# Kernel tuning notes

Hardware: AMD Instinct MI355X
Metric: run time of the kernel (lower is better)

Reference implementation:

```python
import jax, jax.numpy as jnp
import numpy as np

N = 100000   # nodes
E = 1250000  # edges
D = 64       # in = hidden = out channels
LN_EPS = 1e-5
L2_EPS = 1e-12


def setup_inputs() -> dict:
    key = jax.random.key(0)
    ks = jax.random.split(key, 16)
    s = 1.0 / np.sqrt(D)
    inp = {
        "x": jax.random.normal(ks[0], (N, D), jnp.float32),
        "edge_index": jax.random.randint(ks[1], (2, E), 0, N, dtype=jnp.int64),
    }
    for i in range(3):  # SAGEConv i: out = mean_aggr @ Wl + bl + x @ Wr
        inp[f"Wl{i}"] = jax.random.normal(ks[2 + 2 * i], (D, D), jnp.float32) * s
        inp[f"bl{i}"] = jnp.zeros((D,), jnp.float32)
        inp[f"Wr{i}"] = jax.random.normal(ks[3 + 2 * i], (D, D), jnp.float32) * s
    for i in range(2):  # LayerNorm after layers 0,1
        inp[f"g{i}"] = jnp.ones((D,), jnp.float32)
        inp[f"b{i}"] = jnp.zeros((D,), jnp.float32)
    return inp


def _sage_conv(x, src, dst, Wl, bl, Wr):
    # PyG SAGEConv(aggr='mean'): lin_l(mean of neighbor msgs) + lin_r(x)
    agg = jax.ops.segment_sum(x[src], dst, num_segments=N)          # [N, D]
    deg = jax.ops.segment_sum(jnp.ones((src.shape[0],), x.dtype), dst, num_segments=N)
    mean = agg / jnp.maximum(deg, 1.0)[:, None]
    return mean @ Wl + bl + x @ Wr


def _layer_norm(h, g, b):
    mu = jnp.mean(h, axis=-1, keepdims=True)
    var = jnp.mean((h - mu) ** 2, axis=-1, keepdims=True)
    return (h - mu) * jax.lax.rsqrt(var + LN_EPS) * g + b


def reference(x, edge_index, Wl0, bl0, Wr0, Wl1, bl1, Wr1, Wl2, bl2, Wr2, g0, b0, g1, b1):
    src, dst = edge_index[0], edge_index[1]
    Ws = [(Wl0, bl0, Wr0), (Wl1, bl1, Wr1), (Wl2, bl2, Wr2)]
    lns = [(g0, b0), (g1, b1)]
    h = x
    for i in range(3):
        res = h  # residual projections are Identity (equal dims)
        h = _sage_conv(h, src, dst, *Ws[i])
        if i < 2:
            h = _layer_norm(h, *lns[i])
            h = jax.nn.relu(h)
            h = h + res
            # dropout is identity in eval mode
        else:
            h = h + res
    # F.normalize(p=2, dim=1)
    nrm = jnp.sqrt(jnp.sum(h * h, axis=1, keepdims=True))
    return h / jnp.maximum(nrm, L2_EPS)
```

## Files before the change

kernel.cpp:

```cpp
#include <hip/hip_runtime.h>

#define DD   64
#define KK   128
#define XSTR 132
#define BSH  9
#define BNODES 512
#define BCAPSH 13

typedef unsigned int uint32;

__device__ __forceinline__ unsigned short f2bf_rne(float f) {
    uint32 u = __float_as_uint(f);
    u += 0x7fffu + ((u >> 16) & 1u);
    return (unsigned short)(u >> 16);
}
__device__ __forceinline__ float bf_lo(uint32 w) { return __uint_as_float(w << 16); }
__device__ __forceinline__ float bf_hi(uint32 w) { return __uint_as_float(w & 0xffff0000u); }

__global__ __launch_bounds__(256) void cvt_kernel(const float* __restrict__ x,
                                                  unsigned short* __restrict__ xb,
                                                  int n4, int* __restrict__ gCnt) {
    if (blockIdx.x == 0 && threadIdx.x < 256) gCnt[threadIdx.x] = 0;
    int i = blockIdx.x * 256 + threadIdx.x;
    if (i < n4) {
        float4 v = ((const float4*)x)[i];
        ushort4 p;
        p.x = f2bf_rne(v.x); p.y = f2bf_rne(v.y);
        p.z = f2bf_rne(v.z); p.w = f2bf_rne(v.w);
        ((ushort4*)xb)[i] = p;
    }
}

__global__ __launch_bounds__(1024) void bucket_kernel(const int* __restrict__ src,
                                                      const int* __restrict__ dst,
                                                      int* __restrict__ gCnt,
                                                      int2* __restrict__ buf, int E) {
    __shared__ int ldsCnt[256];
    __shared__ int base[256];
    const int t = threadIdx.x;
    if (t < 256) ldsCnt[t] = 0;
    __syncthreads();

    const int e0 = blockIdx.x * 4096;
    int bk[4], rk[4], sv[4], dv[4];
#pragma unroll
    for (int k = 0; k < 4; ++k) {
        int e = e0 + k * 1024 + t;
        bk[k] = -1;
        if (e < E) {
            dv[k] = dst[e];
            sv[k] = src[e];
            bk[k] = dv[k] >> BSH;
            rk[k] = atomicAdd(&ldsCnt[bk[k]], 1);
        }
    }
    __syncthreads();
    if (t < 256 && ldsCnt[t] > 0) base[t] = atomicAdd(&gCnt[t], ldsCnt[t]);
    __syncthreads();
#pragma unroll
    for (int k = 0; k < 4; ++k) {
        if (bk[k] >= 0) {
            int pos = (bk[k] << BCAPSH) + base[bk[k]] + rk[k];
            buf[pos] = make_int2(sv[k], dv[k]);
        }
    }
}

__global__ __launch_bounds__(256) void scan_buckets(const int* __restrict__ gCnt,
                                                    int* __restrict__ csrBase, int NB) {
    __shared__ int s[256];
    int t = threadIdx.x;
    int v = (t < NB) ? gCnt[t] : 0;
    s[t] = v;
    __syncthreads();
    for (int d = 1; d < 256; d <<= 1) {
        int u = (t >= d) ? s[t - d] : 0;
        __syncthreads();
        if (t >= d) s[t] += u;
        __syncthreads();
    }
    if (t < NB) csrBase[t] = s[t] - v;
}

__global__ __launch_bounds__(512) void csr_build(const int2* __restrict__ buf,
                                                 const int* __restrict__ gCnt,
                                                 const int* __restrict__ csrBase,
                                                 int* __restrict__ offsets,
                                                 int* __restrict__ csr, int N, int E) {
    __shared__ int c1[BNODES];
    __shared__ int s[BNODES];
    const int b = blockIdx.x;
    const int t = threadIdx.x;
    c1[t] = 0;
    __syncthreads();

    const int cnt = gCnt[b];
    const int2* bb = buf + ((size_t)b << BCAPSH);
    for (int i = t; i < cnt; i += 512) atomicAdd(&c1[bb[i].y & (BNODES - 1)], 1);
    __syncthreads();

    int v = c1[t];
    s[t] = v;
    __syncthreads();
    for (int d = 1; d < BNODES; d <<= 1) {
        int u = (t >= d) ? s[t - d] : 0;
        __syncthreads();
        if (t >= d) s[t] += u;
        __syncthreads();
    }
    int excl = s[t] - v;
    const int base = csrBase[b];
    const int node = (b << BSH) + t;
    if (node < N) offsets[node] = base + excl;
    if (b == 0 && t == 0) offsets[N] = E;
    __syncthreads();
    s[t] = excl;
    c1[t] = 0;
    __syncthreads();

    for (int i = t; i < cnt; i += 512) {
        int2 e = bb[i];
        int d = e.y & (BNODES - 1);
        int r = atomicAdd(&c1[d], 1);
        csr[base + s[d] + r] = e.x;
    }
}

__global__ __launch_bounds__(256) void aggregate_kernel(
    const unsigned short* __restrict__ hb,
    const int* __restrict__ offsets,
    const int* __restrict__ csr,
    float* __restrict__ agg,
    int N) {
    int node = (blockIdx.x * 256 + threadIdx.x) >> 3;
    if (node >= N) return;
    const int q = threadIdx.x & 7;

    const int off0 = offsets[node];
    const int off1 = offsets[node + 1];

    float a0 = 0.f, a1 = 0.f, a2 = 0.f, a3 = 0.f,
          a4 = 0.f, a5 = 0.f, a6 = 0.f, a7 = 0.f;

    for (int j = off0; j < off1; j += 8) {
        uint4 v[8];
#pragma unroll
        for (int s = 0; s < 8; ++s) {
            uint4 t = make_uint4(0u, 0u, 0u, 0u);
            int idx = j + s;
            if (idx < off1) {
                int sn = __builtin_nontemporal_load(&csr[idx]);
                t = ((const uint4*)(hb + (size_t)sn * DD))[q];
            }
            v[s] = t;
        }
#pragma unroll
        for (int s = 0; s < 8; ++s) {
            a0 += bf_lo(v[s].x); a1 += bf_hi(v[s].x);
            a2 += bf_lo(v[s].y); a3 += bf_hi(v[s].y);
            a4 += bf_lo(v[s].z); a5 += bf_hi(v[s].z);
            a6 += bf_lo(v[s].w); a7 += bf_hi(v[s].w);
        }
    }
    float invd = 1.0f / fmaxf((float)(off1 - off0), 1.0f);
    float4 lo = make_float4(a0 * invd, a1 * invd, a2 * invd, a3 * invd);
    float4 hi = make_float4(a4 * invd, a5 * invd, a6 * invd, a7 * invd);
    *(float4*)(&agg[(size_t)node * DD + q * 8])     = lo;
    *(float4*)(&agg[(size_t)node * DD + q * 8 + 4]) = hi;
}

template <int MODE>
__global__ __launch_bounds__(256) void node_update(
    const float* __restrict__ h,
    const float* __restrict__ mean,
    const float* __restrict__ Wl,
    const float* __restrict__ bl,
    const float* __restrict__ Wr,
    const float* __restrict__ g,
    const float* __restrict__ b,
    float* __restrict__ out,
    unsigned short* __restrict__ outb,
    int nNodes) {
    __shared__ float sW[KK * DD];
    __shared__ float sX[64 * XSTR];
    __shared__ float sbl[DD], sg[DD], sb[DD];

    const int t = threadIdx.x;

    for (int i = t; i < DD * DD; i += 256) {
        sW[i]           = Wl[i];
        sW[DD * DD + i] = Wr[i];
    }
    if (t < DD) {
        sbl[t] = bl[t];
        if (MODE == 0) { sg[t] = g[t]; sb[t] = b[t]; }
    }

    const int nbase = blockIdx.x * 64;

    for (int r = 0; r < 8; ++r) {
        int idx  = r * 256 + t;
        int node = idx >> 5;
        int q    = idx & 31;
        int n    = nbase + node;
        float4 v = make_float4(0.f, 0.f, 0.f, 0.f);
        if (n < nNodes) {
            v = (q < 16) ? ((const float4*)(mean + (size_t)n * DD))[q]
                         : ((const float4*)(h    + (size_t)n * DD))[q - 16];
        }
        *(float4*)(&sX[node * XSTR + q * 4]) = v;
    }
    __syncthreads();

    const int c0 = (t & 15) * 4;
    const int n0 = (t >> 4) * 4;

    float acc[4][4];
#pragma unroll
    for (int i = 0; i < 4; ++i)
#pragma unroll
        for (int j = 0; j < 4; ++j) acc[i][j] = sbl[c0 + j];

#pragma unroll 8
    for (int k = 0; k < KK; ++k) {
        const float4 w = *(const float4*)(&sW[k * DD + c0]);
#pragma unroll
        for (int i = 0; i < 4; ++i) {
            float xv = sX[(n0 + i) * XSTR + k];
            acc[i][0] = fmaf(xv, w.x, acc[i][0]);
            acc[i][1] = fmaf(xv, w.y, acc[i][1]);
            acc[i][2] = fmaf(xv, w.z, acc[i][2]);
            acc[i][3] = fmaf(xv, w.w, acc[i][3]);
        }
    }

    float res[4][4];
#pragma unroll
    for (int i = 0; i < 4; ++i) {
        float4 rv = *(const float4*)(&sX[(n0 + i) * XSTR + 64 + c0]);
        res[i][0] = rv.x; res[i][1] = rv.y; res[i][2] = rv.z; res[i][3] = rv.w;
    }

#pragma unroll
    for (int i = 0; i < 4; ++i) {
        int nn = nbase + n0 + i;
        float4 o;
        if (MODE == 0) {
            float s = acc[i][0] + acc[i][1] + acc[i][2] + acc[i][3];
            s += __shfl_xor(s, 1, 64);
            s += __shfl_xor(s, 2, 64);
            s += __shfl_xor(s, 4, 64);
            s += __shfl_xor(s, 8, 64);
            float mu = s * (1.0f / 64.0f);
            float d0 = acc[i][0] - mu, d1 = acc[i][1] - mu,
                  d2 = acc[i][2] - mu, d3 = acc[i][3] - mu;
            float qq = d0 * d0 + d1 * d1 + d2 * d2 + d3 * d3;
            qq += __shfl_xor(qq, 1, 64);
            qq += __shfl_xor(qq, 2, 64);
            qq += __shfl_xor(qq, 4, 64);
            qq += __shfl_xor(qq, 8, 64);
            float rstd = rsqrtf(qq * (1.0f / 64.0f) + 1e-5f);
            o.x = fmaxf(d0 * rstd * sg[c0 + 0] + sb[c0 + 0], 0.f) + res[i][0];
            o.y = fmaxf(d1 * rstd * sg[c0 + 1] + sb[c0 + 1], 0.f) + res[i][1];
            o.z = fmaxf(d2 * rstd * sg[c0 + 2] + sb[c0 + 2], 0.f) + res[i][2];
            o.w = fmaxf(d3 * rstd * sg[c0 + 3] + sb[c0 + 3], 0.f) + res[i][3];
        } else {
            float y0 = acc[i][0] + res[i][0], y1 = acc[i][1] + res[i][1],
                  y2 = acc[i][2] + res[i][2], y3 = acc[i][3] + res[i][3];
            float qq = y0 * y0 + y1 * y1 + y2 * y2 + y3 * y3;
            qq += __shfl_xor(qq, 1, 64);
            qq += __shfl_xor(qq, 2, 64);
            qq += __shfl_xor(qq, 4, 64);
            qq += __shfl_xor(qq, 8, 64);
            float inv = 1.0f / fmaxf(sqrtf(qq), 1e-12f);
            o.x = y0 * inv; o.y = y1 * inv; o.z = y2 * inv; o.w = y3 * inv;
        }
        if (nn < nNodes) {
            *(float4*)(&out[(size_t)nn * DD + c0]) = o;
            if (MODE == 0) {
                ushort4 p;
                p.x = f2bf_rne(o.x); p.y = f2bf_rne(o.y);
                p.z = f2bf_rne(o.z); p.w = f2bf_rne(o.w);
                *(ushort4*)(&outb[(size_t)nn * DD + c0]) = p;
            }
        }
    }
}

extern "C" void kernel_launch(void* const* d_in, const int* in_sizes, int n_in,
                              void* d_out, int out_size, void* d_ws, size_t ws_size,
                              hipStream_t stream) {
    const float* x   = (const float*)d_in[0];
    const int*   ei  = (const int*)d_in[1];
    const float* Wl0 = (const float*)d_in[2];
    const float* bl0 = (const float*)d_in[3];
    const float* Wr0 = (const float*)d_in[4];
    const float* Wl1 = (const float*)d_in[5];
    const float* bl1 = (const float*)d_in[6];
    const float* Wr1 = (const float*)d_in[7];
    const float* Wl2 = (const float*)d_in[8];
    const float* bl2 = (const float*)d_in[9];
    const float* Wr2 = (const float*)d_in[10];
    const float* g0  = (const float*)d_in[11];
    const float* b0  = (const float*)d_in[12];
    const float* g1  = (const float*)d_in[13];
    const float* b1  = (const float*)d_in[14];

    const int N = in_sizes[0] / DD;
    const int E = in_sizes[1] / 2;
    const int* src = ei;
    const int* dst = ei + E;
    const int NB = (N + BNODES - 1) >> BSH;

    float* A       = (float*)d_ws;
    float* B       = A + (size_t)N * DD;
    float* AGG     = B + (size_t)N * DD;
    int2*  bucketBuf = (int2*)A;
    unsigned short* HB = (unsigned short*)(AGG + (size_t)N * DD);
    int*   offsets = (int*)(HB + (size_t)N * DD);
    int*   gCnt    = offsets + (N + 1);
    int*   csrBase = gCnt + 256;
    int*   csr     = csrBase + 256;
    float* out     = (float*)d_out;

    const int tiles = (N + 63) / 64;
    const int agrid = (N + 31) / 32;
    const int n4    = N * DD / 4;
    const int cgrid = (n4 + 255) / 256;
    const int bgrid = (E + 4095) / 4096;

    cvt_kernel<<<cgrid, 256, 0, stream>>>(x, HB, n4, gCnt);
    bucket_kernel<<<bgrid, 1024, 0, stream>>>(src, dst, gCnt, bucketBuf, E);
    scan_buckets<<<1, 256, 0, stream>>>(gCnt, csrBase, NB);
    csr_build<<<NB, 512, 0, stream>>>(bucketBuf, gCnt, csrBase, offsets, csr, N, E);

    aggregate_kernel<<<agrid, 256, 0, stream>>>(HB, offsets, csr, AGG, N);
    node_update<0><<<tiles, 256, 0, stream>>>(x, AGG, Wl0, bl0, Wr0, g0, b0, A, HB, N);

    aggregate_kernel<<<agrid, 256, 0, stream>>>(HB, offsets, csr, AGG, N);
    node_update<0><<<tiles, 256, 0, stream>>>(A, AGG, Wl1, bl1, Wr1, g1, b1, B, HB, N);

    aggregate_kernel<<<agrid, 256, 0, stream>>>(HB, offsets, csr, AGG, N);
    node_update<1><<<tiles, 256, 0, stream>>>(B, AGG, Wl2, bl2, Wr2, nullptr, nullptr, out, nullptr, N);
}
```

Measured before the change: 373.8 us.

## Use bf16 MFMA in node update and store aggregated means as bf16

```diff
diff --git a/kernel.cpp b/kernel.cpp
--- a/kernel.cpp
+++ b/kernel.cpp
@@ -1,13 +1,14 @@
 #include <hip/hip_runtime.h>
 
 #define DD   64
-#define KK   128
-#define XSTR 132
+#define WSTR 136
 #define BSH  9
 #define BNODES 512
 #define BCAPSH 13
 
 typedef unsigned int uint32;
+typedef __attribute__((ext_vector_type(8))) short short8;
+typedef __attribute__((ext_vector_type(4))) float f32x4;
 
 __device__ __forceinline__ unsigned short f2bf_rne(float f) {
     uint32 u = __float_as_uint(f);
@@ -130,7 +131,7 @@
     const unsigned short* __restrict__ hb,
     const int* __restrict__ offsets,
     const int* __restrict__ csr,
-    float* __restrict__ agg,
+    unsigned short* __restrict__ aggb,
     int N) {
     int node = (blockIdx.x * 256 + threadIdx.x) >> 3;
     if (node >= N) return;
@@ -163,16 +164,21 @@
         }
     }
     float invd = 1.0f / fmaxf((float)(off1 - off0), 1.0f);
-    float4 lo = make_float4(a0 * invd, a1 * invd, a2 * invd, a3 * invd);
-    float4 hi = make_float4(a4 * invd, a5 * invd, a6 * invd, a7 * invd);
-    *(float4*)(&agg[(size_t)node * DD + q * 8])     = lo;
-    *(float4*)(&agg[(size_t)node * DD + q * 8 + 4]) = hi;
+    unsigned short* orow = aggb + (size_t)node * DD + q * 8;
+    ushort4 pa, pb;
+    pa.x = f2bf_rne(a0 * invd); pa.y = f2bf_rne(a1 * invd);
+    pa.z = f2bf_rne(a2 * invd); pa.w = f2bf_rne(a3 * invd);
+    pb.x = f2bf_rne(a4 * invd); pb.y = f2bf_rne(a5 * invd);
+    pb.z = f2bf_rne(a6 * invd); pb.w = f2bf_rne(a7 * invd);
+    *(ushort4*)(orow)     = pa;
+    *(ushort4*)(orow + 4) = pb;
 }
 
 template <int MODE>
-__global__ __launch_bounds__(256) void node_update(
+__global__ __launch_bounds__(256, 4) void node_update(
     const float* __restrict__ h,
-    const float* __restrict__ mean,
+    const unsigned short* __restrict__ meanb,
+    const unsigned short* __restrict__ hb,
     const float* __restrict__ Wl,
     const float* __restrict__ bl,
     const float* __restrict__ Wr,
@@ -181,107 +187,105 @@
     float* __restrict__ out,
     unsigned short* __restrict__ outb,
     int nNodes) {
-    __shared__ float sW[KK * DD];
-    __shared__ float sX[64 * XSTR];
+    __shared__ unsigned short sWt[64 * WSTR];
     __shared__ float sbl[DD], sg[DD], sb[DD];
 
     const int t = threadIdx.x;
 
-    for (int i = t; i < DD * DD; i += 256) {
-        sW[i]           = Wl[i];
-        sW[DD * DD + i] = Wr[i];
+    for (int idx = t; idx < 2 * DD * DD; idx += 256) {
+        int k = idx >> 6, c = idx & 63;
+        float v = (k < DD) ? Wl[idx] : Wr[idx - DD * DD];
+        sWt[c * WSTR + k] = f2bf_rne(v);
     }
     if (t < DD) {
         sbl[t] = bl[t];
         if (MODE == 0) { sg[t] = g[t]; sb[t] = b[t]; }
     }
-
-    const int nbase = blockIdx.x * 64;
-
-    for (int r = 0; r < 8; ++r) {
-        int idx  = r * 256 + t;
-        int node = idx >> 5;
-        int q    = idx & 31;
-        int n    = nbase + node;
-        float4 v = make_float4(0.f, 0.f, 0.f, 0.f);
-        if (n < nNodes) {
-            v = (q < 16) ? ((const float4*)(mean + (size_t)n * DD))[q]
-                         : ((const float4*)(h    + (size_t)n * DD))[q - 16];
-        }
-        *(float4*)(&sX[node * XSTR + q * 4]) = v;
-    }
-    __syncthreads();
-
-    const int c0 = (t & 15) * 4;
-    const int n0 = (t >> 4) * 4;
-
-    float acc[4][4];
-#pragma unroll
-    for (int i = 0; i < 4; ++i)
-#pragma unroll
-        for (int j = 0; j < 4; ++j) acc[i][j] = sbl[c0 + j];
-
-#pragma unroll 8
-    for (int k = 0; k < KK; ++k) {
-        const float4 w = *(const float4*)(&sW[k * DD + c0]);
-#pragma unroll
-        for (int i = 0; i < 4; ++i) {
-            float xv = sX[(n0 + i) * XSTR + k];
-            acc[i][0] = fmaf(xv, w.x, acc[i][0]);
-            acc[i][1] = fmaf(xv, w.y, acc[i][1]);
-            acc[i][2] = fmaf(xv, w.z, acc[i][2]);
-            acc[i][3] = fmaf(xv, w.w, acc[i][3]);
-        }
-    }
-
+    __syncthreads();
+
+    const int wave = t >> 6;
+    const int lane = t & 63;
+    const int quad = lane >> 4;
+    const int n16  = lane & 15;
+    const int nbase = blockIdx.x * 64 + wave * 16;
+
+    const int arow = min(nbase + n16, nNodes - 1);
+    const unsigned short* mrow = meanb + (size_t)arow * DD;
+    const unsigned short* hrow = hb    + (size_t)arow * DD;
+    short8 af[4];
+    af[0] = *(const short8*)(mrow + quad * 8);
+    af[1] = *(const short8*)(mrow + 32 + quad * 8);
+    af[2] = *(const short8*)(hrow + quad * 8);
+    af[3] = *(const short8*)(hrow + 32 + quad * 8);
+
+    const int rbase = nbase + quad * 4;
     float res[4][4];
 #pragma unroll
     for (int i = 0; i < 4; ++i) {
-        float4 rv = *(const float4*)(&sX[(n0 + i) * XSTR + 64 + c0]);
-        res[i][0] = rv.x; res[i][1] = rv.y; res[i][2] = rv.z; res[i][3] = rv.w;
+        int rr = min(rbase + i, nNodes - 1);
+#pragma unroll
+        for (int j = 0; j < 4; ++j)
+            res[i][j] = h[(size_t)rr * DD + j * 16 + n16];
+    }
+
+    f32x4 acc[4];
+#pragma unroll
+    for (int j = 0; j < 4; ++j) {
+        float bv = sbl[j * 16 + n16];
+        acc[j] = (f32x4){bv, bv, bv, bv};
+    }
+
+#pragma unroll
+    for (int s = 0; s < 4; ++s) {
+#pragma unroll
+        for (int j = 0; j < 4; ++j) {
+            short8 bf = *(const short8*)(&sWt[(j * 16 + n16) * WSTR + s * 32 + quad * 8]);
+            acc[j] = __builtin_amdgcn_mfma_f32_16x16x32_bf16(af[s], bf, acc[j], 0, 0, 0);
+        }
     }
 
 #pragma unroll
     for (int i = 0; i < 4; ++i) {
-        int nn = nbase + n0 + i;
-        float4 o;
+        int rr = rbase + i;
+        float o[4];
         if (MODE == 0) {
-            float s = acc[i][0] + acc[i][1] + acc[i][2] + acc[i][3];
-            s += __shfl_xor(s, 1, 64);
-            s += __shfl_xor(s, 2, 64);
-            s += __shfl_xor(s, 4, 64);
-            s += __shfl_xor(s, 8, 64);
-            float mu = s * (1.0f / 64.0f);
-            float d0 = acc[i][0] - mu, d1 = acc[i][1] - mu,
-                  d2 = acc[i][2] - mu, d3 = acc[i][3] - mu;
+            float s4 = acc[0][i] + acc[1][i] + acc[2][i] + acc[3][i];
+            s4 += __shfl_xor(s4, 1, 64);
+            s4 += __shfl_xor(s4, 2, 64);
+            s4 += __shfl_xor(s4, 4, 64);
+            s4 += __shfl_xor(s4, 8, 64);
+            float mu = s4 * (1.0f / 64.0f);
+            float d0 = acc[0][i] - mu, d1 = acc[1][i] - mu,
+                  d2 = acc[2][i] - mu, d3 = acc[3][i] - mu;
             float qq = d0 * d0 + d1 * d1 + d2 * d2 + d3 * d3;
             qq += __shfl_xor(qq, 1, 64);
             qq += __shfl_xor(qq, 2, 64);
             qq += __shfl_xor(qq, 4, 64);
             qq += __shfl_xor(qq, 8, 64);
             float rstd = rsqrtf(qq * (1.0f / 64.0f) + 1e-5f);
-            o.x = fmaxf(d0 * rstd * sg[c0 + 0] + sb[c0 + 0], 0.f) + res[i][0];
-            o.y = fmaxf(d1 * rstd * sg[c0 + 1] + sb[c0 + 1], 0.f) + res[i][1];
-            o.z = fmaxf(d2 * rstd * sg[c0 + 2] + sb[c0 + 2], 0.f) + res[i][2];
-            o.w = fmaxf(d3 * rstd * sg[c0 + 3] + sb[c0 + 3], 0.f) + res[i][3];
+            o[0] = fmaxf(d0 * rstd * sg[0 * 16 + n16] + sb[0 * 16 + n16], 0.f) + res[i][0];
+            o[1] = fmaxf(d1 * rstd * sg[1 * 16 + n16] + sb[1 * 16 + n16], 0.f) + res[i][1];
+            o[2] = fmaxf(d2 * rstd * sg[2 * 16 + n16] + sb[2 * 16 + n16], 0.f) + res[i][2];
+            o[3] = fmaxf(d3 * rstd * sg[3 * 16 + n16] + sb[3 * 16 + n16], 0.f) + res[i][3];
         } else {
-            float y0 = acc[i][0] + res[i][0], y1 = acc[i][1] + res[i][1],
-                  y2 = acc[i][2] + res[i][2], y3 = acc[i][3] + res[i][3];
-            float qq = y0 * y0 + y1 * y1 + y2 * y2 + y3 * y3;
+            o[0] = acc[0][i] + res[i][0];
+            o[1] = acc[1][i] + res[i][1];
+            o[2] = acc[2][i] + res[i][2];
+            o[3] = acc[3][i] + res[i][3];
+            float qq = o[0] * o[0] + o[1] * o[1] + o[2] * o[2] + o[3] * o[3];
             qq += __shfl_xor(qq, 1, 64);
             qq += __shfl_xor(qq, 2, 64);
             qq += __shfl_xor(qq, 4, 64);
             qq += __shfl_xor(qq, 8, 64);
             float inv = 1.0f / fmaxf(sqrtf(qq), 1e-12f);
-            o.x = y0 * inv; o.y = y1 * inv; o.z = y2 * inv; o.w = y3 * inv;
-        }
-        if (nn < nNodes) {
-            *(float4*)(&out[(size_t)nn * DD + c0]) = o;
-            if (MODE == 0) {
-                ushort4 p;
-                p.x = f2bf_rne(o.x); p.y = f2bf_rne(o.y);
-                p.z = f2bf_rne(o.z); p.w = f2bf_rne(o.w);
-                *(ushort4*)(&outb[(size_t)nn * DD + c0]) = p;
+            o[0] *= inv; o[1] *= inv; o[2] *= inv; o[3] *= inv;
+        }
+        if (rr < nNodes) {
+#pragma unroll
+            for (int j = 0; j < 4; ++j) {
+                out[(size_t)rr * DD + j * 16 + n16] = o[j];
+                if (MODE == 0)
+                    outb[(size_t)rr * DD + j * 16 + n16] = f2bf_rne(o[j]);
             }
         }
     }
@@ -314,13 +318,13 @@
 
     float* A       = (float*)d_ws;
     float* B       = A + (size_t)N * DD;
-    float* AGG     = B + (size_t)N * DD;
-    int2*  bucketBuf = (int2*)A;
-    unsigned short* HB = (unsigned short*)(AGG + (size_t)N * DD);
+    unsigned short* AGGB = (unsigned short*)(B + (size_t)N * DD);
+    unsigned short* HB   = AGGB + (size_t)N * DD;
     int*   offsets = (int*)(HB + (size_t)N * DD);
     int*   gCnt    = offsets + (N + 1);
     int*   csrBase = gCnt + 256;
     int*   csr     = csrBase + 256;
+    int2*  bucketBuf = (int2*)A;
     float* out     = (float*)d_out;
 
     const int tiles = (N + 63) / 64;
@@ -334,12 +338,12 @@
     scan_buckets<<<1, 256, 0, stream>>>(gCnt, csrBase, NB);
     csr_build<<<NB, 512, 0, stream>>>(bucketBuf, gCnt, csrBase, offsets, csr, N, E);
 
-    aggregate_kernel<<<agrid, 256, 0, stream>>>(HB, offsets, csr, AGG, N);
-    node_update<0><<<tiles, 256, 0, stream>>>(x, AGG, Wl0, bl0, Wr0, g0, b0, A, HB, N);
-
-    aggregate_kernel<<<agrid, 256, 0, stream>>>(HB, offsets, csr, AGG, N);
-    node_update<0><<<tiles, 256, 0, stream>>>(A, AGG, Wl1, bl1, Wr1, g1, b1, B, HB, N);
-
-    aggregate_kernel<<<agrid, 256, 0, stream>>>(HB, offsets, csr, AGG, N);
-    node_update<1><<<tiles, 256, 0, stream>>>(B, AGG, Wl2, bl2, Wr2, nullptr, nullptr, out, nullptr, N);
-}
+    aggregate_kernel<<<agrid, 256, 0, stream>>>(HB, offsets, csr, AGGB, N);
+    node_update<0><<<tiles, 256, 0, stream>>>(x, AGGB, HB, Wl0, bl0, Wr0, g0, b0, A, HB, N);
+
+    aggregate_kernel<<<agrid, 256, 0, stream>>>(HB, offsets, csr, AGGB, N);
+    node_update<0><<<tiles, 256, 0, stream>>>(A, AGGB, HB, Wl1, bl1, Wr1, g1, b1, B, HB, N);
+
+    aggregate_kernel<<<agrid, 256, 0, stream>>>(HB, offsets, csr, AGGB, N);
+    node_update<1><<<tiles, 256, 0, stream>>>(B, AGGB, HB, Wl2, bl2, Wr2, nullptr, nullptr, out, nullptr, N);
+}
```

Result: faster. 314.2 us (-15.9%).
